# Optimization experiments

Hardware: AMD Instinct MI355X
Metric: run time of the kernel (lower is better)

Reference implementation:

```python
import jax, jax.numpy as jnp
import numpy as np

NUM_HEADS = 16

def setup_inputs() -> dict:
    key = jax.random.key(0)
    ks = jax.random.split(key, 8)
    B, S, D = 2, 2048, 1024
    w = lambda k: jax.random.normal(k, (D, D), dtype=jnp.float32) * 0.02
    return {
        "x": jax.random.normal(ks[0], (B, S, D), dtype=jnp.float32),
        "attn_mask": jnp.zeros((S, S), dtype=jnp.float32),
        "key_padding_mask": jnp.zeros((B, S), dtype=bool),
        "Wq": w(ks[1]), "bq": jnp.zeros((D,), jnp.float32),
        "Wk": w(ks[2]), "bk": jnp.zeros((D,), jnp.float32),
        "Wv": w(ks[3]), "bv": jnp.zeros((D,), jnp.float32),
        "Wg": w(ks[4]), "bg": jnp.full((D,), 0.5, jnp.float32),  # gate_bias_init=0.5
        "Wo": w(ks[5]), "bo": jnp.zeros((D,), jnp.float32),
    }

def reference(x, attn_mask, key_padding_mask, Wq, bq, Wk, bk, Wv, bv, Wg, bg, Wo, bo):
    B, S, D = x.shape
    H = NUM_HEADS
    hd = D // H
    scale = jnp.sqrt(jnp.float32(hd)).astype(x.dtype)

    def split_heads(t):  # (B,S,D) -> (B,H,S,hd)
        return t.reshape(B, S, H, hd).transpose(0, 2, 1, 3)

    q = split_heads(x @ Wq + bq)
    k = split_heads(x @ Wk + bk)
    v = split_heads(x @ Wv + bv)

    scores = jnp.einsum("bhqd,bhkd->bhqk", q, k) / scale
    scores = scores + attn_mask[None, None, :, :]
    scores = jnp.where(key_padding_mask[:, None, None, :], -jnp.inf, scores)

    attn_weights = jax.nn.softmax(scores, axis=-1)          # (B,H,S,S)
    attn_out = jnp.einsum("bhqk,bhkd->bhqd", attn_weights, v)

    gate = jax.nn.sigmoid(x @ Wg + bg)                      # (B,S,D)
    gate = split_heads(gate)                                # (B,H,S,hd)
    attn_out = attn_out * gate

    attn_out = attn_out.transpose(0, 2, 1, 3).reshape(B, S, D)
    output = attn_out @ Wo + bo
    avg_attn = attn_weights.mean(axis=1)                    # (B,S,S)
    return output, avg_attn
```

## Files before the change

kernel.cpp:

```cpp
#include <hip/hip_runtime.h>
#include <hip/hip_bf16.h>

#define LOG2E 1.4426950408889634f

typedef short short8 __attribute__((ext_vector_type(8)));
typedef float floatx4 __attribute__((ext_vector_type(4)));

__device__ __forceinline__ floatx4 mfma16(short8 a, short8 b, floatx4 c) {
    return __builtin_amdgcn_mfma_f32_16x16x32_bf16(a, b, c, 0, 0, 0);
}

__device__ __forceinline__ float fexp2(float x) { return __builtin_amdgcn_exp2f(x); }

__device__ __forceinline__ short f2bf(float f) {
    unsigned u = __builtin_bit_cast(unsigned, f);
    u += 0x7FFFu + ((u >> 16) & 1u);
    return (short)(u >> 16);
}
__device__ __forceinline__ unsigned bfpack(float a, float b) {
    unsigned ua = __builtin_bit_cast(unsigned, a) + 0x8000u;
    unsigned ub = __builtin_bit_cast(unsigned, b) + 0x8000u;
    return __builtin_amdgcn_perm(ub, ua, 0x07060302u);
}
__device__ __forceinline__ float bf2f(short s) {
    unsigned u = ((unsigned)(unsigned short)s) << 16;
    return __builtin_bit_cast(float, u);
}

__device__ __forceinline__ void glds16(const void* g, void* l) {
    __builtin_amdgcn_global_load_lds(
        (const __attribute__((address_space(1))) void*)g,
        (__attribute__((address_space(3))) void*)l, 16, 0, 0);
}

__device__ __forceinline__ short8 cvt8(const float* __restrict__ p) {
    float4 a = *reinterpret_cast<const float4*>(p);
    float4 b = *reinterpret_cast<const float4*>(p + 4);
    short8 r;
    r[0] = f2bf(a.x); r[1] = f2bf(a.y); r[2] = f2bf(a.z); r[3] = f2bf(a.w);
    r[4] = f2bf(b.x); r[5] = f2bf(b.y); r[6] = f2bf(b.z); r[7] = f2bf(b.w);
    return r;
}

__global__ __launch_bounds__(256) void cvt_x_kernel(
    const float* __restrict__ in, short* __restrict__ out, int n8)
{
    int i = blockIdx.x * blockDim.x + threadIdx.x;
    if (i < n8)
        *reinterpret_cast<short8*>(out + (size_t)i * 8) = cvt8(in + (size_t)i * 8);
}

__global__ __launch_bounds__(256) void cvt_wt_kernel(
    const float* __restrict__ W0, const float* __restrict__ W1,
    const float* __restrict__ W2, const float* __restrict__ W3,
    const float* __restrict__ W4, short* __restrict__ Wt)
{
    __shared__ short T[64 * 66];
    const int w = blockIdx.z;
    const float* W = (w == 0) ? W0 : (w == 1) ? W1 : (w == 2) ? W2 : (w == 3) ? W3 : W4;
    short* dst = Wt + (size_t)w * 1024 * 1024;
    const int kb = blockIdx.y * 64, nb = blockIdx.x * 64;
    const int t = threadIdx.x;
    const int r = t >> 2, c4 = (t & 3) * 16;
    *reinterpret_cast<short8*>(T + r * 66 + c4)     = cvt8(W + (size_t)(kb + r) * 1024 + nb + c4);
    *reinterpret_cast<short8*>(T + r * 66 + c4 + 8) = cvt8(W + (size_t)(kb + r) * 1024 + nb + c4 + 8);
    __syncthreads();
    short8 o0, o1;
    #pragma unroll
    for (int j = 0; j < 8; ++j) o0[j] = T[(c4 + j) * 66 + r];
    #pragma unroll
    for (int j = 0; j < 8; ++j) o1[j] = T[(c4 + 8 + j) * 66 + r];
    *reinterpret_cast<short8*>(dst + (size_t)(nb + r) * 1024 + kb + c4)     = o0;
    *reinterpret_cast<short8*>(dst + (size_t)(nb + r) * 1024 + kb + c4 + 8) = o1;
}

__global__ __launch_bounds__(256) void flag_scan(
    const float* __restrict__ amask, const unsigned char* __restrict__ kpm,
    int* __restrict__ flag)
{
    const int i = blockIdx.x * 256 + threadIdx.x;
    const float4* a4 = reinterpret_cast<const float4*>(amask);
    float4 v0 = a4[(size_t)i * 2];
    float4 v1 = a4[(size_t)i * 2 + 1];
    bool nz = (v0.x != 0.f) | (v0.y != 0.f) | (v0.z != 0.f) | (v0.w != 0.f)
            | (v1.x != 0.f) | (v1.y != 0.f) | (v1.z != 0.f) | (v1.w != 0.f);
    if (blockIdx.x == 0) {
        const uint4* k4 = reinterpret_cast<const uint4*>(kpm);
        uint4 kv = k4[threadIdx.x];
        nz |= ((kv.x | kv.y | kv.z | kv.w) != 0u);
    }
    if (__ballot(nz) && ((threadIdx.x & 63) == 0)) atomicOr(flag, 1);
}

__global__ __launch_bounds__(256) void mask_prep(
    const float* __restrict__ amask, const unsigned char* __restrict__ kpm,
    float* __restrict__ Mc, const int* __restrict__ flag)
{
    if (*flag == 0) return;
    const int b = blockIdx.z, q = blockIdx.y;
    const int p0 = threadIdx.x * 8;
    float o[8];
    #pragma unroll
    for (int i = 0; i < 8; ++i) {
        int p = p0 + i;
        int j = (p & ~31) | ((p >> 1) & 15) | ((p & 1) << 4);
        unsigned char kb = kpm[b * 2048 + j];
        float a = amask[(size_t)q * 2048 + j];
        o[i] = a * LOG2E + (kb ? -1.0e30f : 0.f);
    }
    float* dst = Mc + ((size_t)b * 2048 + q) * 2048 + p0;
    *reinterpret_cast<float4*>(dst)     = make_float4(o[0], o[1], o[2], o[3]);
    *reinterpret_cast<float4*>(dst + 4) = make_float4(o[4], o[5], o[6], o[7]);
}

__device__ __forceinline__ void gemm_core256p(
    const short* __restrict__ A, const short* __restrict__ Wt,
    int mbase, int nbase, short* Asm, short* Bsm, floatx4 (&acc)[8][4])
{
    const int tid = threadIdx.x;
    const int lane = tid & 63, wid = tid >> 6;
    const int L15 = lane & 15, g = lane >> 4;
    const int wrow = (wid >> 2) * 128, wcol = (wid & 3) * 64;

    const int rl4 = lane >> 2, c4 = lane & 3;
    const int R0 = wid * 32;
    const short* aG = A  + (size_t)(mbase + R0 + rl4) * 1024 + c4 * 8;
    const short* bG = Wt + (size_t)(nbase + R0 + rl4) * 1024 + c4 * 8;

#define STAGE(t_) do {                                                        \
        const int sl_ = (t_) & 3;                                             \
        glds16(aG + (size_t)(t_) * 32,         Asm + sl_ * 8192 + R0 * 32);   \
        glds16(aG + (size_t)(t_) * 32 + 16384, Asm + sl_ * 8192 + R0 * 32 + 512); \
        glds16(bG + (size_t)(t_) * 32,         Bsm + sl_ * 8192 + R0 * 32);   \
        glds16(bG + (size_t)(t_) * 32 + 16384, Bsm + sl_ * 8192 + R0 * 32 + 512); \
    } while (0)

#define BARRIER_SB() do {                                                     \
        __builtin_amdgcn_sched_barrier(0);                                    \
        __builtin_amdgcn_s_barrier();                                         \
        __builtin_amdgcn_sched_barrier(0);                                    \
    } while (0)

    STAGE(0); STAGE(1);
    asm volatile("s_waitcnt vmcnt(4)" ::: "memory");
    BARRIER_SB();

    for (int t = 0; t < 32; ++t) {
        const int sl = t & 3;
        const short* Ab = Asm + sl * 8192;
        const short* Bb = Bsm + sl * 8192;
        short8 bf[4], af[4];
        #pragma unroll
        for (int nt = 0; nt < 4; ++nt)
            bf[nt] = *reinterpret_cast<const short8*>(Bb + (wcol + nt * 16 + L15) * 32 + g * 8);
        #pragma unroll
        for (int mt = 0; mt < 4; ++mt)
            af[mt] = *reinterpret_cast<const short8*>(Ab + (wrow + mt * 16 + L15) * 32 + g * 8);
        #pragma unroll
        for (int mt = 0; mt < 4; ++mt)
            #pragma unroll
            for (int nt = 0; nt < 4; ++nt)
                acc[mt][nt] = mfma16(af[mt], bf[nt], acc[mt][nt]);

        if (t + 2 < 32) STAGE(t + 2);

        #pragma unroll
        for (int mt = 0; mt < 4; ++mt)
            af[mt] = *reinterpret_cast<const short8*>(Ab + (wrow + 64 + mt * 16 + L15) * 32 + g * 8);
        #pragma unroll
        for (int mt = 0; mt < 4; ++mt)
            #pragma unroll
            for (int nt = 0; nt < 4; ++nt)
                acc[mt + 4][nt] = mfma16(af[mt], bf[nt], acc[mt + 4][nt]);

        if (t + 2 < 32)      asm volatile("s_waitcnt vmcnt(4)" ::: "memory");
        else if (t + 1 < 32) asm volatile("s_waitcnt vmcnt(0)" ::: "memory");
        BARRIER_SB();
    }

#undef STAGE
#undef BARRIER_SB
}

__device__ __forceinline__ void gemm_core(
    const short* __restrict__ A, const short* __restrict__ Wt,
    int mbase, int nbase, short* Asm, short* Bsm, floatx4 (&acc)[4][4])
{
    const int tid = threadIdx.x;
    const int lane = tid & 63, wid = tid >> 6;
    const int L15 = lane & 15, g = lane >> 4;
    const int wm = (wid >> 1) * 64, wn = (wid & 1) * 64;

    const int rowoff = lane >> 3;
    const int choff = ((lane & 7) ^ rowoff) * 8;
    const short* aP = A  + (size_t)(mbase + wid * 32 + rowoff) * 1024 + choff;
    const short* bP = Wt + (size_t)(nbase + wid * 32 + rowoff) * 1024 + choff;
    short* aL = Asm + wid * 2048;
    short* bL = Bsm + wid * 2048;

    const int xb = L15 & 7;
    const int s0 = (g ^ xb) * 8;
    const int s1 = ((g ^ 4) ^ xb) * 8;

    for (int kb = 0; kb < 1024; kb += 64) {
        __syncthreads();
        #pragma unroll
        for (int j = 0; j < 4; ++j) glds16(aP + kb + j * 8192, aL + j * 512);
        #pragma unroll
        for (int j = 0; j < 4; ++j) glds16(bP + kb + j * 8192, bL + j * 512);
        __syncthreads();
        #pragma unroll
        for (int ks = 0; ks < 2; ++ks) {
            const int so = ks ? s1 : s0;
            short8 af[4], bf[4];
            #pragma unroll
            for (int mt = 0; mt < 4; ++mt)
                af[mt] = *reinterpret_cast<const short8*>(Asm + (wm + mt * 16 + L15) * 64 + so);
            #pragma unroll
            for (int nt = 0; nt < 4; ++nt)
                bf[nt] = *reinterpret_cast<const short8*>(Bsm + (wn + nt * 16 + L15) * 64 + so);
            #pragma unroll
            for (int mt = 0; mt < 4; ++mt)
                #pragma unroll
                for (int nt = 0; nt < 4; ++nt)
                    acc[mt][nt] = mfma16(af[mt], bf[nt], acc[mt][nt]);
        }
    }
}

__global__ __launch_bounds__(512) void qkvg_gemm(
    const short* __restrict__ A, const short* __restrict__ Wt5,
    const float* __restrict__ b0, const float* __restrict__ b1,
    const float* __restrict__ b2, const float* __restrict__ b3,
    short* __restrict__ dQ, short* __restrict__ dK,
    short* __restrict__ dV, short* __restrict__ dG)
{
    __shared__ short Asm[4 * 8192];
    __shared__ short Bsm[4 * 8192];

    const int wg = blockIdx.x;
    const int swz = (wg & 7) * 32 + (wg >> 3);
    const int z = swz >> 6;
    const int rem = swz & 63;
    const int mbase = (rem >> 2) * 256, nbase = (rem & 3) * 256;

    floatx4 acc[8][4] = {};
    gemm_core256p(A, Wt5 + (size_t)z * 1048576, mbase, nbase, Asm, Bsm, acc);

    const int lane = threadIdx.x & 63, wid = threadIdx.x >> 6;
    const int L15 = lane & 15, g = lane >> 4;
    const int wrow = (wid >> 2) * 128, wcol = (wid & 3) * 64;
    const float* bz = (z == 0) ? b0 : (z == 1) ? b1 : (z == 2) ? b2 : b3;
    short* dst = (z == 0) ? dQ : (z == 1) ? dK : (z == 2) ? dV : dG;

    float bvv[4];
    #pragma unroll
    for (int nt = 0; nt < 4; ++nt) bvv[nt] = bz[nbase + wcol + nt * 16 + L15];

    if (z <= 1) {
        const float qsc = (z == 0) ? 0.125f * LOG2E : 1.0f;
        #pragma unroll
        for (int mt = 0; mt < 8; ++mt) {
            #pragma unroll
            for (int r = 0; r < 4; ++r) {
                int row = mbase + wrow + mt * 16 + g * 4 + r;
                int bb = row >> 11, s = row & 2047;
                #pragma unroll
                for (int nt = 0; nt < 4; ++nt) {
                    int col = nbase + wcol + nt * 16 + L15;
                    int hh = col >> 6, dh = col & 63;
                    dst[(((size_t)bb * 16 + hh) * 2048 + s) * 64 + dh] =
                        f2bf((acc[mt][nt][r] + bvv[nt]) * qsc);
                }
            }
        }
    } else if (z == 2) {
        #pragma unroll
        for (int nt = 0; nt < 4; ++nt) {
            int col = nbase + wcol + nt * 16 + L15;
            int hh = col >> 6, dh = col & 63;
            #pragma unroll
            for (int mt = 0; mt < 8; ++mt) {
                #pragma unroll
                for (int r = 0; r < 4; ++r) {
                    int row = mbase + wrow + mt * 16 + g * 4 + r;
                    int bb = row >> 11, s = row & 2047;
                    int sp = (s & ~31) | ((s & 15) << 1) | ((s >> 4) & 1);
                    dst[(((size_t)bb * 16 + hh) * 64 + dh) * 2048 + sp] =
                        f2bf(acc[mt][nt][r] + bvv[nt]);
                }
            }
        }
    } else {
        #pragma unroll
        for (int mt = 0; mt < 8; ++mt) {
            #pragma unroll
            for (int r = 0; r < 4; ++r) {
                int row = mbase + wrow + mt * 16 + g * 4 + r;
                #pragma unroll
                for (int nt = 0; nt < 4; ++nt) {
                    int col = nbase + wcol + nt * 16 + L15;
                    float e = fexp2(-(acc[mt][nt][r] + bvv[nt]) * LOG2E);
                    dst[(size_t)row * 1024 + col] = f2bf(__builtin_amdgcn_rcpf(1.0f + e));
                }
            }
        }
    }
}

__global__ __launch_bounds__(256) void out_gemm(
    const short* __restrict__ A, const short* __restrict__ Wt,
    const float* __restrict__ bias, float* __restrict__ out)
{
    __shared__ short Asm[128 * 64];
    __shared__ short Bsm[128 * 64];
    const int mbase = blockIdx.y * 128, nbase = blockIdx.x * 128;
    floatx4 acc[4][4] = {};
    gemm_core(A, Wt, mbase, nbase, Asm, Bsm, acc);

    const int lane = threadIdx.x & 63, wid = threadIdx.x >> 6;
    const int L15 = lane & 15, g = lane >> 4;
    const int wm = (wid >> 1) * 64, wn = (wid & 1) * 64;
    #pragma unroll
    for (int nt = 0; nt < 4; ++nt) {
        int col = nbase + wn + nt * 16 + L15;
        float bv = bias[col];
        #pragma unroll
        for (int mt = 0; mt < 4; ++mt)
            #pragma unroll
            for (int r = 0; r < 4; ++r) {
                int row = mbase + wm + mt * 16 + g * 4 + r;
                out[(size_t)row * 1024 + col] = acc[mt][nt][r] + bv;
            }
    }
}

template<bool MASKED>
__device__ __forceinline__ void flash_body(
    const short* __restrict__ Q, const short* __restrict__ K,
    const short* __restrict__ Vt, const short* __restrict__ G,
    const float* __restrict__ Mc, short* __restrict__ att,
    float* __restrict__ inv_l,
    short* Ksm, short* Vsm, short* Psm)
{
    const int tid = threadIdx.x;
    const int lane = tid & 63, wid = tid >> 6;
    const int L15 = lane & 15, g = lane >> 4;
    const int b = blockIdx.z, h = blockIdx.x;
    const int bh = b * 16 + h;
    const int qb = blockIdx.y * 128 + wid * 16;

    short8 aq0 = *reinterpret_cast<const short8*>(Q + ((size_t)bh * 2048 + qb + L15) * 64 + g * 8);
    short8 aq1 = *reinterpret_cast<const short8*>(Q + ((size_t)bh * 2048 + qb + L15) * 64 + 32 + g * 8);

    floatx4 O[4] = {};
    float l_r[4] = {0.f, 0.f, 0.f, 0.f};

    const int krow = lane >> 3;
    const int kch  = ((lane & 7) ^ krow) * 8;
    const bool isK = wid < 4;
    const int sw = isK ? wid : (wid - 4);
    const short* gP;
    if (isK) {
        gP = K + ((size_t)bh * 2048 + sw * 16 + krow) * 64 + kch;
    } else {
        const int vsc = (lane & 7) ^ krow;
        const int vhd = sw * 16 + 2 * krow + (vsc >> 2);
        gP = Vt + ((size_t)bh * 64 + vhd) * 2048 + (vsc & 3) * 8;
    }

    const int x7 = L15 & 7;
    const int sk0 = (g ^ x7) * 8, sk1 = ((g ^ 4) ^ x7) * 8;
    const int sv = (((L15 & 1) * 4 + g) ^ ((L15 >> 1) & 7)) * 8;
    const int vp = (L15 >> 1) * 64;

    short* Pw = Psm + wid * 1152;

    const float* mcP[4];
    float2 mc0[4], mc1[4];
    if (MASKED) {
        #pragma unroll
        for (int r = 0; r < 4; ++r) {
            mcP[r] = Mc + ((size_t)b * 2048 + qb + g * 4 + r) * 2048 + 2 * L15;
            mc0[r] = *reinterpret_cast<const float2*>(mcP[r]);
            mc1[r] = *reinterpret_cast<const float2*>(mcP[r] + 32);
        }
    }

    if (isK) {
        glds16(gP,       Ksm + sw * 1024);
        glds16(gP + 512, Ksm + sw * 1024 + 512);
    } else {
        glds16(gP,      Vsm + sw * 512);
        glds16(gP + 32, Vsm + 2048 + sw * 512);
    }

    for (int kb = 0; kb < 2048; kb += 64) {
        const int cur = (kb >> 6) & 1;
        __syncthreads();
        const int nb = kb + 64;
        const bool more = nb < 2048;
        float2 nmc0[4], nmc1[4];
        if (more) {
            if (isK) {
                glds16(gP + (size_t)nb * 64,       Ksm + (cur ^ 1) * 4096 + sw * 1024);
                glds16(gP + (size_t)nb * 64 + 512, Ksm + (cur ^ 1) * 4096 + sw * 1024 + 512);
            } else {
                glds16(gP + nb,      Vsm + (cur ^ 1) * 4096 + sw * 512);
                glds16(gP + nb + 32, Vsm + (cur ^ 1) * 4096 + 2048 + sw * 512);
            }
            if (MASKED) {
                #pragma unroll
                for (int r = 0; r < 4; ++r) {
                    nmc0[r] = *reinterpret_cast<const float2*>(mcP[r] + nb);
                    nmc1[r] = *reinterpret_cast<const float2*>(mcP[r] + nb + 32);
                }
            }
        }

        const short* Kb = Ksm + cur * 4096;
        floatx4 s[4];
        #pragma unroll
        for (int kt = 0; kt < 4; ++kt) {
            s[kt] = {};
            s[kt] = mfma16(aq0, *reinterpret_cast<const short8*>(Kb + (kt * 16 + L15) * 64 + sk0), s[kt]);
            s[kt] = mfma16(aq1, *reinterpret_cast<const short8*>(Kb + (kt * 16 + L15) * 64 + sk1), s[kt]);
        }

        #pragma unroll
        for (int r = 0; r < 4; ++r) {
            float e0 = fexp2(MASKED ? s[0][r] + mc0[r].x : s[0][r]);
            float e1 = fexp2(MASKED ? s[1][r] + mc0[r].y : s[1][r]);
            float e2 = fexp2(MASKED ? s[2][r] + mc1[r].x : s[2][r]);
            float e3 = fexp2(MASKED ? s[3][r] + mc1[r].y : s[3][r]);
            l_r[r] += (e0 + e1) + (e2 + e3);
            *reinterpret_cast<unsigned*>(&Pw[(g * 4 + r) * 72 + 2 * L15])      = bfpack(e0, e1);
            *reinterpret_cast<unsigned*>(&Pw[(g * 4 + r) * 72 + 32 + 2 * L15]) = bfpack(e2, e3);
        }
        short8 ap0 = *reinterpret_cast<const short8*>(&Pw[L15 * 72 + g * 8]);
        short8 ap1 = *reinterpret_cast<const short8*>(&Pw[L15 * 72 + 32 + g * 8]);
        const short* Vb0 = Vsm + cur * 4096;
        const short* Vb1 = Vb0 + 2048;
        #pragma unroll
        for (int t = 0; t < 4; ++t) {
            O[t] = mfma16(ap0, *reinterpret_cast<const short8*>(Vb0 + t * 512 + vp + sv), O[t]);
            O[t] = mfma16(ap1, *reinterpret_cast<const short8*>(Vb1 + t * 512 + vp + sv), O[t]);
        }

        if (MASKED && more) {
            #pragma unroll
            for (int r = 0; r < 4; ++r) { mc0[r] = nmc0[r]; mc1[r] = nmc1[r]; }
        }
    }

    float inv[4];
    #pragma unroll
    for (int r = 0; r < 4; ++r) {
        float ls = l_r[r];
        ls += __shfl_xor(ls, 1);
        ls += __shfl_xor(ls, 2);
        ls += __shfl_xor(ls, 4);
        ls += __shfl_xor(ls, 8);
        inv[r] = 1.0f / ls;
        if (L15 == 0) inv_l[(size_t)bh * 2048 + qb + g * 4 + r] = inv[r];
    }
    #pragma unroll
    for (int t = 0; t < 4; ++t) {
        int col = h * 64 + t * 16 + L15;
        #pragma unroll
        for (int r = 0; r < 4; ++r) {
            size_t qr = qb + g * 4 + r;
            float gt = bf2f(G[((size_t)b * 2048 + qr) * 1024 + col]);
            att[((size_t)b * 2048 + qr) * 1024 + col] = f2bf(O[t][r] * inv[r] * gt);
        }
    }
}

__global__ __launch_bounds__(512, 4) void flash_attn(
    const short* __restrict__ Q, const short* __restrict__ K,
    const short* __restrict__ Vt, const short* __restrict__ G,
    const float* __restrict__ Mc, const int* __restrict__ flag,
    short* __restrict__ att, float* __restrict__ inv_l)
{
    __shared__ short Ksm[2 * 4096];
    __shared__ short Vsm[2 * 4096];
    __shared__ short Psm[8 * 1152];
    if (*flag)
        flash_body<true>(Q, K, Vt, G, Mc, att, inv_l, Ksm, Vsm, Psm);
    else
        flash_body<false>(Q, K, Vt, G, Mc, att, inv_l, Ksm, Vsm, Psm);
}

template<bool MASKED>
__device__ __forceinline__ void avg_body(
    const short* __restrict__ Q, const short* __restrict__ K,
    const float* __restrict__ inv_l, float* mca, short* KsmBase)
{
    const int tid = threadIdx.x;
    const int lane = tid & 63, wid = tid >> 6;
    const int L15 = lane & 15, g = lane >> 4;
    const int b = blockIdx.z;
    const int qb = blockIdx.y * 64 + wid * 16;
    const int ks = blockIdx.x * 128;

    float pm[4][2][4];
    if (MASKED) {
        #pragma unroll
        for (int c = 0; c < 4; ++c)
            #pragma unroll
            for (int r = 0; r < 4; ++r) {
                size_t qr = qb + g * 4 + r;
                float2 m = *reinterpret_cast<const float2*>(
                    mca + ((size_t)b * 2048 + qr) * 2048 + ks + c * 32 + 2 * L15);
                pm[c][0][r] = m.x;
                pm[c][1][r] = m.y;
            }
    }
    float av[4][2][4] = {};

    const int rowoff = lane >> 3;
    const int choff = ((lane & 7) ^ rowoff) * 8;
    const int x7 = L15 & 7;
    const int sk0 = (g ^ x7) * 8, sk1 = ((g ^ 4) ^ x7) * 8;
    short* kL[2] = { KsmBase + wid * 2048, KsmBase + 8192 + wid * 2048 };

    {
        const short* p = K + ((size_t)(b * 16) * 2048 + ks + wid * 32 + rowoff) * 64 + choff;
        #pragma unroll
        for (int j = 0; j < 4; ++j) glds16(p + j * 512, kL[0] + j * 512);
    }
    short8 aq0 = *reinterpret_cast<const short8*>(Q + ((size_t)(b * 16) * 2048 + qb + L15) * 64 + g * 8);
    short8 aq1 = *reinterpret_cast<const short8*>(Q + ((size_t)(b * 16) * 2048 + qb + L15) * 64 + 32 + g * 8);
    float iv[4];
    #pragma unroll
    for (int r = 0; r < 4; ++r) iv[r] = inv_l[(size_t)(b * 16) * 2048 + qb + g * 4 + r];

    for (int h = 0; h < 16; ++h) {
        __syncthreads();
        short8 naq0, naq1;
        float niv[4];
        if (h < 15) {
            int nbh = b * 16 + h + 1;
            const short* p = K + ((size_t)nbh * 2048 + ks + wid * 32 + rowoff) * 64 + choff;
            #pragma unroll
            for (int j = 0; j < 4; ++j) glds16(p + j * 512, kL[(h + 1) & 1] + j * 512);
            naq0 = *reinterpret_cast<const short8*>(Q + ((size_t)nbh * 2048 + qb + L15) * 64 + g * 8);
            naq1 = *reinterpret_cast<const short8*>(Q + ((size_t)nbh * 2048 + qb + L15) * 64 + 32 + g * 8);
            #pragma unroll
            for (int r = 0; r < 4; ++r) niv[r] = inv_l[(size_t)nbh * 2048 + qb + g * 4 + r];
        }

        const short* Kb = KsmBase + (h & 1) * 8192;
        #pragma unroll
        for (int c = 0; c < 4; ++c) {
            const short* kbase = Kb + c * 32 * 64;
            floatx4 s0 = {}, s1 = {};
            s0 = mfma16(aq0, *reinterpret_cast<const short8*>(kbase + L15 * 64 + sk0), s0);
            s0 = mfma16(aq1, *reinterpret_cast<const short8*>(kbase + L15 * 64 + sk1), s0);
            s1 = mfma16(aq0, *reinterpret_cast<const short8*>(kbase + (16 + L15) * 64 + sk0), s1);
            s1 = mfma16(aq1, *reinterpret_cast<const short8*>(kbase + (16 + L15) * 64 + sk1), s1);
            #pragma unroll
            for (int r = 0; r < 4; ++r) {
                av[c][0][r] += fexp2(MASKED ? s0[r] + pm[c][0][r] : s0[r]) * iv[r];
                av[c][1][r] += fexp2(MASKED ? s1[r] + pm[c][1][r] : s1[r]) * iv[r];
            }
        }
        if (h < 15) {
            aq0 = naq0; aq1 = naq1;
            #pragma unroll
            for (int r = 0; r < 4; ++r) iv[r] = niv[r];
        }
    }
    #pragma unroll
    for (int c = 0; c < 4; ++c)
        #pragma unroll
        for (int t = 0; t < 2; ++t)
            #pragma unroll
            for (int r = 0; r < 4; ++r) {
                size_t qr = qb + g * 4 + r;
                int col = ks + c * 32 + t * 16 + L15;
                mca[((size_t)b * 2048 + qr) * 2048 + col] = av[c][t][r] * 0.0625f;
            }
}

__global__ __launch_bounds__(256) void avg_attn_kernel(
    const short* __restrict__ Q, const short* __restrict__ K,
    const float* __restrict__ inv_l, float* mca, const int* __restrict__ flag)
{
    __shared__ short Ksm[2 * 128 * 64];
    if (*flag)
        avg_body<true>(Q, K, inv_l, mca, Ksm);
    else
        avg_body<false>(Q, K, inv_l, mca, Ksm);
}

extern "C" void kernel_launch(void* const* d_in, const int* in_sizes, int n_in,
                              void* d_out, int out_size, void* d_ws, size_t ws_size,
                              hipStream_t stream)
{
    const float* x  = (const float*)d_in[0];
    const float* amask = (const float*)d_in[1];
    const unsigned char* kpm = (const unsigned char*)d_in[2];
    const float* Wq = (const float*)d_in[3];
    const float* bq = (const float*)d_in[4];
    const float* Wk = (const float*)d_in[5];
    const float* bk = (const float*)d_in[6];
    const float* Wv = (const float*)d_in[7];
    const float* bv = (const float*)d_in[8];
    const float* Wg = (const float*)d_in[9];
    const float* bg = (const float*)d_in[10];
    const float* Wo = (const float*)d_in[11];
    const float* bo = (const float*)d_in[12];

    char* ws = (char*)d_ws;
    const size_t MB = 1u << 20;
    short* Xb    = (short*)(ws);
    short* Att   = Xb;
    short* Qw    = (short*)(ws + 8 * MB);
    short* Kw    = (short*)(ws + 16 * MB);
    short* Vt    = (short*)(ws + 24 * MB);
    short* Gw    = (short*)(ws + 32 * MB);
    short* Wt    = (short*)(ws + 40 * MB);
    float* stats = (float*)(ws + 50 * MB);
    int*   flagp = (int*)(ws + 50 * MB + 262144);

    float* outp = (float*)d_out;
    float* avgp = (float*)d_out + 4194304;

    hipMemsetAsync(flagp, 0, sizeof(int), stream);

    flag_scan<<<2048, 256, 0, stream>>>(amask, kpm, flagp);

    cvt_x_kernel<<<2048, 256, 0, stream>>>(x, Xb, 524288);
    cvt_wt_kernel<<<dim3(16, 16, 5), 256, 0, stream>>>(Wq, Wk, Wv, Wg, Wo, Wt);
    mask_prep<<<dim3(1, 2048, 2), 256, 0, stream>>>(amask, kpm, avgp, flagp);

    qkvg_gemm<<<256, 512, 0, stream>>>(Xb, Wt, bq, bk, bv, bg, Qw, Kw, Vt, Gw);

    flash_attn<<<dim3(16, 16, 2), 512, 0, stream>>>(Qw, Kw, Vt, Gw, avgp, flagp, Att, stats);

    avg_attn_kernel<<<dim3(16, 32, 2), 256, 0, stream>>>(Qw, Kw, stats, avgp, flagp);

    out_gemm<<<dim3(8, 32), 256, 0, stream>>>(Att, Wt + 4 * 1048576, bo, outp);
}
```

Before: 269.2 us.

## Process two 16-row query tiles per wave in flash attention with 256-thread blocks

```diff
diff --git a/kernel.cpp b/kernel.cpp
--- a/kernel.cpp
+++ b/kernel.cpp
@@ -348,24 +348,26 @@
     const int L15 = lane & 15, g = lane >> 4;
     const int b = blockIdx.z, h = blockIdx.x;
     const int bh = b * 16 + h;
-    const int qb = blockIdx.y * 128 + wid * 16;
-
-    short8 aq0 = *reinterpret_cast<const short8*>(Q + ((size_t)bh * 2048 + qb + L15) * 64 + g * 8);
-    short8 aq1 = *reinterpret_cast<const short8*>(Q + ((size_t)bh * 2048 + qb + L15) * 64 + 32 + g * 8);
-
-    floatx4 O[4] = {};
-    float l_r[4] = {0.f, 0.f, 0.f, 0.f};
+    const int qb = blockIdx.y * 128 + wid * 32;
+
+    short8 aq0a = *reinterpret_cast<const short8*>(Q + ((size_t)bh * 2048 + qb + L15) * 64 + g * 8);
+    short8 aq1a = *reinterpret_cast<const short8*>(Q + ((size_t)bh * 2048 + qb + L15) * 64 + 32 + g * 8);
+    short8 aq0b = *reinterpret_cast<const short8*>(Q + ((size_t)bh * 2048 + qb + 16 + L15) * 64 + g * 8);
+    short8 aq1b = *reinterpret_cast<const short8*>(Q + ((size_t)bh * 2048 + qb + 16 + L15) * 64 + 32 + g * 8);
+
+    floatx4 Oa[4] = {}, Ob[4] = {};
+    float la[4] = {0.f, 0.f, 0.f, 0.f}, lb[4] = {0.f, 0.f, 0.f, 0.f};
 
     const int krow = lane >> 3;
     const int kch  = ((lane & 7) ^ krow) * 8;
-    const bool isK = wid < 4;
-    const int sw = isK ? wid : (wid - 4);
+    const bool isK = wid < 2;
+    const int sw = isK ? wid : (wid - 2);
     const short* gP;
     if (isK) {
-        gP = K + ((size_t)bh * 2048 + sw * 16 + krow) * 64 + kch;
+        gP = K + ((size_t)bh * 2048 + sw * 32 + krow) * 64 + kch;
     } else {
         const int vsc = (lane & 7) ^ krow;
-        const int vhd = sw * 16 + 2 * krow + (vsc >> 2);
+        const int vhd = sw * 32 + 2 * krow + (vsc >> 2);
         gP = Vt + ((size_t)bh * 64 + vhd) * 2048 + (vsc & 3) * 8;
     }
 
@@ -374,25 +376,31 @@
     const int sv = (((L15 & 1) * 4 + g) ^ ((L15 >> 1) & 7)) * 8;
     const int vp = (L15 >> 1) * 64;
 
-    short* Pw = Psm + wid * 1152;
-
-    const float* mcP[4];
-    float2 mc0[4], mc1[4];
+    short* Pw = Psm + wid * 2304;
+
+    const float* mcPa[4];
+    float2 mc0a[4], mc1a[4], mc0b[4], mc1b[4];
     if (MASKED) {
         #pragma unroll
         for (int r = 0; r < 4; ++r) {
-            mcP[r] = Mc + ((size_t)b * 2048 + qb + g * 4 + r) * 2048 + 2 * L15;
-            mc0[r] = *reinterpret_cast<const float2*>(mcP[r]);
-            mc1[r] = *reinterpret_cast<const float2*>(mcP[r] + 32);
+            mcPa[r] = Mc + ((size_t)b * 2048 + qb + g * 4 + r) * 2048 + 2 * L15;
+            mc0a[r] = *reinterpret_cast<const float2*>(mcPa[r]);
+            mc1a[r] = *reinterpret_cast<const float2*>(mcPa[r] + 32);
+            mc0b[r] = *reinterpret_cast<const float2*>(mcPa[r] + 16 * 2048);
+            mc1b[r] = *reinterpret_cast<const float2*>(mcPa[r] + 16 * 2048 + 32);
         }
     }
 
     if (isK) {
-        glds16(gP,       Ksm + sw * 1024);
-        glds16(gP + 512, Ksm + sw * 1024 + 512);
+        #pragma unroll
+        for (int j = 0; j < 4; ++j)
+            glds16(gP + j * 512, Ksm + sw * 2048 + j * 512);
     } else {
-        glds16(gP,      Vsm + sw * 512);
-        glds16(gP + 32, Vsm + 2048 + sw * 512);
+        #pragma unroll
+        for (int j = 0; j < 2; ++j) {
+            glds16(gP + j * 32768,      Vsm + sw * 1024 + j * 512);
+            glds16(gP + j * 32768 + 32, Vsm + 2048 + sw * 1024 + j * 512);
+        }
     }
 
     for (int kb = 0; kb < 2048; kb += 64) {
@@ -400,83 +408,121 @@
         __syncthreads();
         const int nb = kb + 64;
         const bool more = nb < 2048;
-        float2 nmc0[4], nmc1[4];
+        float2 nmc0a[4], nmc1a[4], nmc0b[4], nmc1b[4];
         if (more) {
+            const int nbuf = (cur ^ 1) * 4096;
             if (isK) {
-                glds16(gP + (size_t)nb * 64,       Ksm + (cur ^ 1) * 4096 + sw * 1024);
-                glds16(gP + (size_t)nb * 64 + 512, Ksm + (cur ^ 1) * 4096 + sw * 1024 + 512);
+                #pragma unroll
+                for (int j = 0; j < 4; ++j)
+                    glds16(gP + (size_t)nb * 64 + j * 512, Ksm + nbuf + sw * 2048 + j * 512);
             } else {
-                glds16(gP + nb,      Vsm + (cur ^ 1) * 4096 + sw * 512);
-                glds16(gP + nb + 32, Vsm + (cur ^ 1) * 4096 + 2048 + sw * 512);
+                #pragma unroll
+                for (int j = 0; j < 2; ++j) {
+                    glds16(gP + nb + j * 32768,      Vsm + nbuf + sw * 1024 + j * 512);
+                    glds16(gP + nb + j * 32768 + 32, Vsm + nbuf + 2048 + sw * 1024 + j * 512);
+                }
             }
             if (MASKED) {
                 #pragma unroll
                 for (int r = 0; r < 4; ++r) {
-                    nmc0[r] = *reinterpret_cast<const float2*>(mcP[r] + nb);
-                    nmc1[r] = *reinterpret_cast<const float2*>(mcP[r] + nb + 32);
+                    nmc0a[r] = *reinterpret_cast<const float2*>(mcPa[r] + nb);
+                    nmc1a[r] = *reinterpret_cast<const float2*>(mcPa[r] + nb + 32);
+                    nmc0b[r] = *reinterpret_cast<const float2*>(mcPa[r] + 16 * 2048 + nb);
+                    nmc1b[r] = *reinterpret_cast<const float2*>(mcPa[r] + 16 * 2048 + nb + 32);
                 }
             }
         }
 
         const short* Kb = Ksm + cur * 4096;
-        floatx4 s[4];
+        floatx4 sa[4], sb[4];
         #pragma unroll
         for (int kt = 0; kt < 4; ++kt) {
-            s[kt] = {};
-            s[kt] = mfma16(aq0, *reinterpret_cast<const short8*>(Kb + (kt * 16 + L15) * 64 + sk0), s[kt]);
-            s[kt] = mfma16(aq1, *reinterpret_cast<const short8*>(Kb + (kt * 16 + L15) * 64 + sk1), s[kt]);
+            short8 kf0 = *reinterpret_cast<const short8*>(Kb + (kt * 16 + L15) * 64 + sk0);
+            short8 kf1 = *reinterpret_cast<const short8*>(Kb + (kt * 16 + L15) * 64 + sk1);
+            sa[kt] = {};
+            sa[kt] = mfma16(aq0a, kf0, sa[kt]);
+            sa[kt] = mfma16(aq1a, kf1, sa[kt]);
+            sb[kt] = {};
+            sb[kt] = mfma16(aq0b, kf0, sb[kt]);
+            sb[kt] = mfma16(aq1b, kf1, sb[kt]);
         }
 
         #pragma unroll
         for (int r = 0; r < 4; ++r) {
-            float e0 = fexp2(MASKED ? s[0][r] + mc0[r].x : s[0][r]);
-            float e1 = fexp2(MASKED ? s[1][r] + mc0[r].y : s[1][r]);
-            float e2 = fexp2(MASKED ? s[2][r] + mc1[r].x : s[2][r]);
-            float e3 = fexp2(MASKED ? s[3][r] + mc1[r].y : s[3][r]);
-            l_r[r] += (e0 + e1) + (e2 + e3);
+            float e0 = fexp2(MASKED ? sa[0][r] + mc0a[r].x : sa[0][r]);
+            float e1 = fexp2(MASKED ? sa[1][r] + mc0a[r].y : sa[1][r]);
+            float e2 = fexp2(MASKED ? sa[2][r] + mc1a[r].x : sa[2][r]);
+            float e3 = fexp2(MASKED ? sa[3][r] + mc1a[r].y : sa[3][r]);
+            la[r] += (e0 + e1) + (e2 + e3);
             *reinterpret_cast<unsigned*>(&Pw[(g * 4 + r) * 72 + 2 * L15])      = bfpack(e0, e1);
             *reinterpret_cast<unsigned*>(&Pw[(g * 4 + r) * 72 + 32 + 2 * L15]) = bfpack(e2, e3);
-        }
-        short8 ap0 = *reinterpret_cast<const short8*>(&Pw[L15 * 72 + g * 8]);
-        short8 ap1 = *reinterpret_cast<const short8*>(&Pw[L15 * 72 + 32 + g * 8]);
+            float f0 = fexp2(MASKED ? sb[0][r] + mc0b[r].x : sb[0][r]);
+            float f1 = fexp2(MASKED ? sb[1][r] + mc0b[r].y : sb[1][r]);
+            float f2 = fexp2(MASKED ? sb[2][r] + mc1b[r].x : sb[2][r]);
+            float f3 = fexp2(MASKED ? sb[3][r] + mc1b[r].y : sb[3][r]);
+            lb[r] += (f0 + f1) + (f2 + f3);
+            *reinterpret_cast<unsigned*>(&Pw[(16 + g * 4 + r) * 72 + 2 * L15])      = bfpack(f0, f1);
+            *reinterpret_cast<unsigned*>(&Pw[(16 + g * 4 + r) * 72 + 32 + 2 * L15]) = bfpack(f2, f3);
+        }
+        short8 ap0a = *reinterpret_cast<const short8*>(&Pw[L15 * 72 + g * 8]);
+        short8 ap1a = *reinterpret_cast<const short8*>(&Pw[L15 * 72 + 32 + g * 8]);
+        short8 ap0b = *reinterpret_cast<const short8*>(&Pw[(16 + L15) * 72 + g * 8]);
+        short8 ap1b = *reinterpret_cast<const short8*>(&Pw[(16 + L15) * 72 + 32 + g * 8]);
         const short* Vb0 = Vsm + cur * 4096;
         const short* Vb1 = Vb0 + 2048;
         #pragma unroll
         for (int t = 0; t < 4; ++t) {
-            O[t] = mfma16(ap0, *reinterpret_cast<const short8*>(Vb0 + t * 512 + vp + sv), O[t]);
-            O[t] = mfma16(ap1, *reinterpret_cast<const short8*>(Vb1 + t * 512 + vp + sv), O[t]);
+            short8 vf0 = *reinterpret_cast<const short8*>(Vb0 + t * 512 + vp + sv);
+            short8 vf1 = *reinterpret_cast<const short8*>(Vb1 + t * 512 + vp + sv);
+            Oa[t] = mfma16(ap0a, vf0, Oa[t]);
+            Oa[t] = mfma16(ap1a, vf1, Oa[t]);
+            Ob[t] = mfma16(ap0b, vf0, Ob[t]);
+            Ob[t] = mfma16(ap1b, vf1, Ob[t]);
         }
 
         if (MASKED && more) {
             #pragma unroll
-            for (int r = 0; r < 4; ++r) { mc0[r] = nmc0[r]; mc1[r] = nmc1[r]; }
-        }
-    }
-
-    float inv[4];
+            for (int r = 0; r < 4; ++r) {
+                mc0a[r] = nmc0a[r]; mc1a[r] = nmc1a[r];
+                mc0b[r] = nmc0b[r]; mc1b[r] = nmc1b[r];
+            }
+        }
+    }
+
+    float inva[4], invb[4];
     #pragma unroll
     for (int r = 0; r < 4; ++r) {
-        float ls = l_r[r];
+        float ls = la[r];
         ls += __shfl_xor(ls, 1);
         ls += __shfl_xor(ls, 2);
         ls += __shfl_xor(ls, 4);
         ls += __shfl_xor(ls, 8);
-        inv[r] = 1.0f / ls;
-        if (L15 == 0) inv_l[(size_t)bh * 2048 + qb + g * 4 + r] = inv[r];
+        inva[r] = 1.0f / ls;
+        if (L15 == 0) inv_l[(size_t)bh * 2048 + qb + g * 4 + r] = inva[r];
+        float lt = lb[r];
+        lt += __shfl_xor(lt, 1);
+        lt += __shfl_xor(lt, 2);
+        lt += __shfl_xor(lt, 4);
+        lt += __shfl_xor(lt, 8);
+        invb[r] = 1.0f / lt;
+        if (L15 == 0) inv_l[(size_t)bh * 2048 + qb + 16 + g * 4 + r] = invb[r];
     }
     #pragma unroll
     for (int t = 0; t < 4; ++t) {
         int col = h * 64 + t * 16 + L15;
         #pragma unroll
         for (int r = 0; r < 4; ++r) {
-            size_t qr = qb + g * 4 + r;
-            float gt = bf2f(G[((size_t)b * 2048 + qr) * 1024 + col]);
-            att[((size_t)b * 2048 + qr) * 1024 + col] = f2bf(O[t][r] * inv[r] * gt);
-        }
-    }
-}
-
-__global__ __launch_bounds__(512, 4) void flash_attn(
+            size_t qra = qb + g * 4 + r;
+            float gta = bf2f(G[((size_t)b * 2048 + qra) * 1024 + col]);
+            att[((size_t)b * 2048 + qra) * 1024 + col] = f2bf(Oa[t][r] * inva[r] * gta);
+            size_t qrb = qb + 16 + g * 4 + r;
+            float gtb = bf2f(G[((size_t)b * 2048 + qrb) * 1024 + col]);
+            att[((size_t)b * 2048 + qrb) * 1024 + col] = f2bf(Ob[t][r] * invb[r] * gtb);
+        }
+    }
+}
+
+__global__ __launch_bounds__(256, 2) void flash_attn(
     const short* __restrict__ Q, const short* __restrict__ K,
     const short* __restrict__ Vt, const short* __restrict__ G,
     const float* __restrict__ Mc, const int* __restrict__ flag,
@@ -484,7 +530,7 @@
 {
     __shared__ short Ksm[2 * 4096];
     __shared__ short Vsm[2 * 4096];
-    __shared__ short Psm[8 * 1152];
+    __shared__ short Psm[4 * 2304];
     if (*flag)
         flash_body<true>(Q, K, Vt, G, Mc, att, inv_l, Ksm, Vsm, Psm);
     else
@@ -637,7 +683,7 @@
 
     qkvg_gemm<<<256, 512, 0, stream>>>(Xb, Wt, bq, bk, bv, bg, Qw, Kw, Vt, Gw);
 
-    flash_attn<<<dim3(16, 16, 2), 512, 0, stream>>>(Qw, Kw, Vt, Gw, avgp, flagp, Att, stats);
+    flash_attn<<<dim3(16, 16, 2), 256, 0, stream>>>(Qw, Kw, Vt, Gw, avgp, flagp, Att, stats);
 
     avg_attn_kernel<<<dim3(16, 32, 2), 256, 0, stream>>>(Qw, Kw, stats, avgp, flagp);
 
```

Result: no change. 266.1 us (-1.2%).
